# Kernel optimization log

Hardware: AMD Instinct MI355X
Metric: run time of the kernel (lower is better)

## Reference

```python
import jax, jax.numpy as jnp
import numpy as np

BATCH, FRAMES, DIM = 64, 2048, 128
BINS = 1024


def setup_inputs() -> dict:
    key = jax.random.key(0)
    kx, ke = jax.random.split(key)
    x = jax.random.normal(kx, (BATCH, FRAMES, DIM), dtype=jnp.float32)
    embed = jax.random.normal(ke, (BINS, DIM), dtype=jnp.float32)
    return {"x": x, "embed": embed}


def reference(x, embed):
    shape = x.shape
    # preprocess: flatten all leading dims -> [N, D]
    flat = x.reshape(-1, shape[-1])
    # quantize: negative squared euclidean distance, argmax == nearest code
    x_sq = jnp.sum(flat * flat, axis=1, keepdims=True)          # [N, 1]
    e_sq = jnp.sum(embed * embed, axis=1)[None, :]               # [1, BINS]
    dist = -(x_sq - 2.0 * flat @ embed.T + e_sq)                 # [N, BINS]
    embed_ind = jnp.argmax(dist, axis=-1)                        # [N]
    # postprocess: reshape indices to leading dims
    embed_ind = embed_ind.reshape(shape[:-1])                    # [B, T]
    # dequantize: embedding gather
    quantize = embed[embed_ind]                                  # [B, T, D]
    return quantize, embed_ind
```

## Files before the change

### kernel.cpp

```cpp
#include <hip/hip_runtime.h>


#define N_ROWS (64 * 2048)
#define DIM 128
#define BINS 1024
#define MARGIN 0.10f

typedef __attribute__((ext_vector_type(8))) _Float16 half8;
typedef __attribute__((ext_vector_type(4))) float f32x4;

__device__ __forceinline__ void glds16(const void* g, void* l) {
    __builtin_amdgcn_global_load_lds((const __attribute__((address_space(1))) char*)g,
                                     (__attribute__((address_space(3))) char*)l, 16, 0, 0);
}

__global__ __launch_bounds__(256) void prep_kernel(const float* __restrict__ embed,
                                                   _Float16* __restrict__ e_img,
                                                   float* __restrict__ esq_g,
                                                   int* __restrict__ counter) {
    int bin = blockIdx.x * 256 + threadIdx.x;
    if (bin == 0) *counter = 0;
    const float4* e4 = (const float4*)(embed + (size_t)bin * DIM);
    int c = bin >> 8, b = bin & 255;
    float s = 0.f;
#pragma unroll
    for (int g = 0; g < 16; ++g) {
        float4 v0 = e4[2 * g], v1 = e4[2 * g + 1];
        s += v0.x * v0.x + v0.y * v0.y + v0.z * v0.z + v0.w * v0.w;
        s += v1.x * v1.x + v1.y * v1.y + v1.z * v1.z + v1.w * v1.w;
        float f[8] = {v0.x, v0.y, v0.z, v0.w, v1.x, v1.y, v1.z, v1.w};
        half8 H;
#pragma unroll
        for (int j = 0; j < 8; ++j) H[j] = (_Float16)f[j];
        int ks = g >> 2, g2 = g & 3;
        size_t off = ((size_t)(c * 4 + ks) << 14) + (size_t)b * 64 + 16 * (g2 ^ ((b >> 2) & 3));
        *(half8*)((char*)e_img + off) = H;
    }
    esq_g[bin] = s;
}

__global__ __launch_bounds__(1024) __attribute__((amdgpu_waves_per_eu(4, 4)))
void vq_mfma_kernel(const float* __restrict__ x,
                    const _Float16* __restrict__ e_img,
                    const float* __restrict__ esq_g,
                    const float* __restrict__ embed,
                    float* __restrict__ out_idx,
                    float* __restrict__ out_q,
                    int* __restrict__ list,
                    int* __restrict__ counter) {
    __shared__ __align__(16) char smem[53248];
    float* esq_s = (float*)(smem + 49152);

    const int t = threadIdx.x;
    const int wv = t >> 6, lane = t & 63, q = lane >> 4, L15 = lane & 15;
    const int h = wv >> 2, bq = wv & 3;
    const int R0 = blockIdx.x * 128;

    {
        esq_s[t] = esq_g[t];
        const float4* xg = (const float4*)(x + (size_t)R0 * DIM);
#pragma unroll
        for (int qq = 0; qq < 2; ++qq) {
            int G = qq * 1024 + t;
            int row = G >> 4, g = G & 15;
            float4 v0 = xg[row * 32 + 2 * g];
            float4 v1 = xg[row * 32 + 2 * g + 1];
            float f[8] = {v0.x, v0.y, v0.z, v0.w, v1.x, v1.y, v1.z, v1.w};
            half8 H;
#pragma unroll
            for (int j = 0; j < 8; ++j) H[j] = (_Float16)f[j];
            int off = row * 256 + 16 * (g ^ (row & 7));
            *(half8*)(smem + off) = H;
        }
    }
    __syncthreads();

    half8 bh[4][2];
    const int rbase = (32 * h + L15) * 256;
#pragma unroll
    for (int ks = 0; ks < 4; ++ks) {
        const int sB = 16 * ((((ks << 2) | q)) ^ (L15 & 7));
#pragma unroll
        for (int nt = 0; nt < 2; ++nt)
            bh[ks][nt] = *(const half8*)(smem + rbase + nt * 4096 + sB);
    }
    __syncthreads();

    const int aOff = (64 * bq + L15) * 64 + 16 * (q ^ ((L15 >> 2) & 3));

    {
        const char* src = (const char*)e_img;
        const int off = wv << 10;
#pragma unroll
        for (int st = 0; st < 2; ++st)
            glds16(src + ((size_t)st << 14) + off + lane * 16, smem + st * 16384 + off);
        asm volatile("s_waitcnt vmcnt(1)" ::: "memory");
    }
    __builtin_amdgcn_s_barrier();
    asm volatile("" ::: "memory");

    float best[2], sec[2];
    int bidx[2];
#pragma unroll
    for (int nt = 0; nt < 2; ++nt) { best[nt] = -3.4e38f; sec[nt] = -3.4e38f; bidx[nt] = 0; }

    for (int c = 0; c < 4; ++c) {
        f32x4 acc[4][2];
#pragma unroll
        for (int mt = 0; mt < 4; ++mt) {
            f32x4 e2v = *(const f32x4*)&esq_s[256 * c + 64 * bq + 16 * mt + 4 * q];
            f32x4 init;
#pragma unroll
            for (int r = 0; r < 4; ++r) init[r] = -0.5f * e2v[r];
            acc[mt][0] = init;
            acc[mt][1] = init;
        }

#pragma unroll
        for (int s = 0; s < 4; ++s) {
            const int gs = c * 4 + s;
            if (gs < 14) {
                const char* src = (const char*)e_img + ((size_t)(gs + 2) << 14);
                char* dst = smem + ((gs + 2) % 3) * 16384;
                const int off = wv << 10;
                glds16(src + off + lane * 16, dst + off);
            }
            const char* buf = smem + (gs % 3) * 16384;
            half8 a[4];
#pragma unroll
            for (int mt = 0; mt < 4; ++mt)
                a[mt] = *(const half8*)(buf + aOff + mt * 1024);
#pragma unroll
            for (int mt = 0; mt < 4; ++mt)
#pragma unroll
                for (int nt = 0; nt < 2; ++nt)
                    acc[mt][nt] = __builtin_amdgcn_mfma_f32_16x16x32_f16(a[mt], bh[s][nt], acc[mt][nt], 0, 0, 0);
            if (gs < 14) {
                asm volatile("s_waitcnt vmcnt(1)" ::: "memory");
            } else if (gs == 14) {
                asm volatile("s_waitcnt vmcnt(0)" ::: "memory");
            }
            __builtin_amdgcn_s_barrier();
            asm volatile("" ::: "memory");
        }

#pragma unroll
        for (int mt = 0; mt < 4; ++mt)
#pragma unroll
            for (int r = 0; r < 4; ++r) {
                int bin = 256 * c + 64 * bq + 16 * mt + 4 * q + r;
#pragma unroll
                for (int nt = 0; nt < 2; ++nt) {
                    float sc = acc[mt][nt][r];
                    bool gt = sc > best[nt];
                    sec[nt] = __builtin_amdgcn_fmed3f(sc, best[nt], sec[nt]);
                    best[nt] = gt ? sc : best[nt];
                    bidx[nt] = gt ? bin : bidx[nt];
                }
            }
    }

#pragma unroll
    for (int nt = 0; nt < 2; ++nt) {
        for (int off = 16; off <= 32; off <<= 1) {
            float ob = __shfl_xor(best[nt], off);
            float os = __shfl_xor(sec[nt], off);
            int oi = __shfl_xor(bidx[nt], off);
            if (ob > best[nt]) { sec[nt] = fmaxf(best[nt], os); best[nt] = ob; bidx[nt] = oi; }
            else sec[nt] = fmaxf(sec[nt], ob);
        }
    }
    __syncthreads();
    float* sv = (float*)smem;
    int* fidx = (int*)(smem + 8192);
    if (q == 0) {
#pragma unroll
        for (int nt = 0; nt < 2; ++nt) {
            int base = (wv * 32 + 16 * nt + L15) * 3;
            sv[base] = best[nt]; sv[base + 1] = sec[nt];
            ((int*)sv)[base + 2] = bidx[nt];
        }
    }
    __syncthreads();
    if (t < 128) {
        int hh = t >> 5, r32 = t & 31;
        int base0 = ((4 * hh) * 32 + r32) * 3;
        float b0 = sv[base0], s0 = sv[base0 + 1];
        int i0 = ((int*)sv)[base0 + 2];
        for (int w = 1; w < 4; ++w) {
            int base = ((4 * hh + w) * 32 + r32) * 3;
            float ob = sv[base], os = sv[base + 1];
            int oi = ((int*)sv)[base + 2];
            if (ob > b0) { s0 = fmaxf(b0, os); b0 = ob; i0 = oi; }
            else s0 = fmaxf(s0, ob);
        }
        out_idx[R0 + t] = (float)i0;
        fidx[t] = i0;
        if (b0 - s0 < 0.5f * MARGIN) {
            int pos = atomicAdd(counter, 1);
            list[pos] = R0 + t;
        }
    }
    __syncthreads();

    {
        const float4* eg = (const float4*)embed;
        float4* og = (float4*)(out_q + (size_t)R0 * DIM);
#pragma unroll
        for (int i = 0; i < 4; ++i) {
            int f = i * 1024 + t;
            int r = f >> 5, cc = f & 31;
            og[(size_t)r * 32 + cc] = eg[(size_t)fidx[r] * 32 + cc];
        }
    }
}

#define SWB(r, c4) ((r) * 128 + 4 * ((c4) ^ ((r) & 31)))
__global__ __launch_bounds__(256) void refine_kernel(const float* __restrict__ x,
                                                     const float* __restrict__ embed,
                                                     const float* __restrict__ esq_g,
                                                     float* __restrict__ out_idx,
                                                     float* __restrict__ out_q,
                                                     const int* __restrict__ list,
                                                     const int* __restrict__ counter) {
    __shared__ float xr[16 * 128];
    __shared__ float bs[64 * 128];
    __shared__ int rowbuf[16];
    __shared__ int ridx[16];

    const int t = threadIdx.x;
    const int tx = t & 63;
    const int ty = t >> 6;
    const int F = *counter;

    for (int tile = blockIdx.x; tile * 16 < F; tile += gridDim.x) {
        const int base = tile * 16;
        __syncthreads();
        if (t < 16) rowbuf[t] = list[min(base + t, F - 1)];
        __syncthreads();
#pragma unroll
        for (int i = 0; i < 2; ++i) {
            int f = i * 256 + t;
            int r = f >> 5, cc = f & 31;
            float4 v = ((const float4*)(x + (size_t)rowbuf[r] * DIM))[cc];
            *(float4*)&xr[r * 128 + cc * 4] = v;
        }

        float bb[4]; int bi[4];
#pragma unroll
        for (int rr = 0; rr < 4; ++rr) { bb[rr] = -3.4e38f; bi[rr] = 0; }

        for (int chunk = 0; chunk < 16; ++chunk) {
            __syncthreads();
            const float4* eg = (const float4*)(embed + (size_t)chunk * 64 * DIM);
#pragma unroll
            for (int i = 0; i < 8; ++i) {
                int f = i * 256 + t;
                int r = f >> 5, cc = f & 31;
                float4 v = eg[f];
                *(float4*)&bs[SWB(r, cc)] = v;
            }
            __syncthreads();

            float acc[4];
#pragma unroll
            for (int rr = 0; rr < 4; ++rr) acc[rr] = 0.f;
#pragma unroll 8
            for (int k4 = 0; k4 < 32; ++k4) {
                float4 b = *(const float4*)&bs[SWB(tx, k4)];
#pragma unroll
                for (int rr = 0; rr < 4; ++rr) {
                    float4 a = *(const float4*)&xr[(4 * ty + rr) * 128 + k4 * 4];
                    acc[rr] = fmaf(a.x, b.x, acc[rr]);
                    acc[rr] = fmaf(a.y, b.y, acc[rr]);
                    acc[rr] = fmaf(a.z, b.z, acc[rr]);
                    acc[rr] = fmaf(a.w, b.w, acc[rr]);
                }
            }
            const int bin = chunk * 64 + tx;
            const float e2 = esq_g[bin];
#pragma unroll
            for (int rr = 0; rr < 4; ++rr) {
                float sc = 2.f * acc[rr] - e2;
                if (sc > bb[rr]) { bb[rr] = sc; bi[rr] = bin; }
            }
        }

        __syncthreads();
        float* vals = bs;
        int* idxs = (int*)(bs + 1024);
#pragma unroll
        for (int rr = 0; rr < 4; ++rr) {
            vals[(4 * ty + rr) * 64 + tx] = bb[rr];
            idxs[(4 * ty + rr) * 64 + tx] = bi[rr];
        }
        __syncthreads();
        if (t < 16) {
            float bv = vals[t * 64];
            int bix = idxs[t * 64];
            for (int j = 1; j < 64; ++j) {
                float v = vals[t * 64 + j];
                int id = idxs[t * 64 + j];
                if (v > bv || (v == bv && id < bix)) { bv = v; bix = id; }
            }
            ridx[t] = bix;
            if (base + t < F) out_idx[rowbuf[t]] = (float)bix;
        }
        __syncthreads();
        {
            const float4* eg = (const float4*)embed;
#pragma unroll
            for (int i = 0; i < 2; ++i) {
                int f = i * 256 + t;
                int r = f >> 5, cc = f & 31;
                float4* og = (float4*)(out_q + (size_t)rowbuf[r] * DIM);
                og[cc] = eg[(size_t)ridx[r] * 32 + cc];
            }
        }
    }
}

extern "C" void kernel_launch(void* const* d_in, const int* in_sizes, int n_in,
                              void* d_out, int out_size, void* d_ws, size_t ws_size,
                              hipStream_t stream) {
    const float* x = (const float*)d_in[0];
    const float* embed = (const float*)d_in[1];
    float* out_q = (float*)d_out;
    float* out_idx = out_q + (size_t)N_ROWS * DIM;
    char* wsb = (char*)d_ws;
    _Float16* e_img = (_Float16*)wsb;
    float* esq_g = (float*)(wsb + (16 << 14));
    int* counter = (int*)(wsb + (16 << 14) + 4096);
    int* list = (int*)(wsb + (16 << 14) + 4096 + 128);

    prep_kernel<<<BINS / 256, 256, 0, stream>>>(embed, e_img, esq_g, counter);
    vq_mfma_kernel<<<N_ROWS / 128, 1024, 0, stream>>>(x, e_img, esq_g, embed,
                                                      out_idx, out_q, list, counter);
    refine_kernel<<<1024, 256, 0, stream>>>(x, embed, esq_g, out_idx, out_q, list, counter);
}
```

Baseline: 253.7 us.

## Load codebook fragments directly from global memory instead of LDS pipeline

Reorders the fp16 codebook image so that each wave's MFMA A-operand fragment sits contiguously in global memory, and reads those fragments straight into registers instead of staging them through a triple-buffered LDS ring with barriers. Blocks shrink from 1024 threads and 128 rows to 512 threads and 64 rows with much less shared memory, and the forced waves-per-EU attribute is removed. This drops per-step barriers and LDS traffic and should raise occupancy, at the cost of relying on L2/L1 for codebook reuse and exposing global-load latency to the MFMA loop.

```diff
diff --git a/kernel.cpp b/kernel.cpp
--- a/kernel.cpp
+++ b/kernel.cpp
@@ -8,11 +8,6 @@
 
 typedef __attribute__((ext_vector_type(8))) _Float16 half8;
 typedef __attribute__((ext_vector_type(4))) float f32x4;
-
-__device__ __forceinline__ void glds16(const void* g, void* l) {
-    __builtin_amdgcn_global_load_lds((const __attribute__((address_space(1))) char*)g,
-                                     (__attribute__((address_space(3))) char*)l, 16, 0, 0);
-}
 
 __global__ __launch_bounds__(256) void prep_kernel(const float* __restrict__ embed,
                                                    _Float16* __restrict__ e_img,
@@ -22,6 +17,7 @@
     if (bin == 0) *counter = 0;
     const float4* e4 = (const float4*)(embed + (size_t)bin * DIM);
     int c = bin >> 8, b = bin & 255;
+    int bq = b >> 6, mt = (b >> 4) & 3, L15 = b & 15;
     float s = 0.f;
 #pragma unroll
     for (int g = 0; g < 16; ++g) {
@@ -32,14 +28,14 @@
         half8 H;
 #pragma unroll
         for (int j = 0; j < 8; ++j) H[j] = (_Float16)f[j];
-        int ks = g >> 2, g2 = g & 3;
-        size_t off = ((size_t)(c * 4 + ks) << 14) + (size_t)b * 64 + 16 * (g2 ^ ((b >> 2) & 3));
+        int gs = c * 4 + (g >> 2), q = g & 3;
+        size_t off = ((size_t)(((gs * 4 + bq) * 4) + mt) << 10) + (size_t)((q * 16 + L15) << 4);
         *(half8*)((char*)e_img + off) = H;
     }
     esq_g[bin] = s;
 }
 
-__global__ __launch_bounds__(1024) __attribute__((amdgpu_waves_per_eu(4, 4)))
+__global__ __launch_bounds__(512)
 void vq_mfma_kernel(const float* __restrict__ x,
                     const _Float16* __restrict__ e_img,
                     const float* __restrict__ esq_g,
@@ -48,20 +44,21 @@
                     float* __restrict__ out_q,
                     int* __restrict__ list,
                     int* __restrict__ counter) {
-    __shared__ __align__(16) char smem[53248];
-    float* esq_s = (float*)(smem + 49152);
+    __shared__ __align__(16) char smem[20480];
+    float* esq_s = (float*)(smem + 16384);
 
     const int t = threadIdx.x;
     const int wv = t >> 6, lane = t & 63, q = lane >> 4, L15 = lane & 15;
     const int h = wv >> 2, bq = wv & 3;
-    const int R0 = blockIdx.x * 128;
+    const int R0 = blockIdx.x * 64;
 
     {
         esq_s[t] = esq_g[t];
+        esq_s[t + 512] = esq_g[t + 512];
         const float4* xg = (const float4*)(x + (size_t)R0 * DIM);
 #pragma unroll
         for (int qq = 0; qq < 2; ++qq) {
-            int G = qq * 1024 + t;
+            int G = qq * 512 + t;
             int row = G >> 4, g = G & 15;
             float4 v0 = xg[row * 32 + 2 * g];
             float4 v1 = xg[row * 32 + 2 * g + 1];
@@ -84,20 +81,8 @@
         for (int nt = 0; nt < 2; ++nt)
             bh[ks][nt] = *(const half8*)(smem + rbase + nt * 4096 + sB);
     }
-    __syncthreads();
-
-    const int aOff = (64 * bq + L15) * 64 + 16 * (q ^ ((L15 >> 2) & 3));
-
-    {
-        const char* src = (const char*)e_img;
-        const int off = wv << 10;
-#pragma unroll
-        for (int st = 0; st < 2; ++st)
-            glds16(src + ((size_t)st << 14) + off + lane * 16, smem + st * 16384 + off);
-        asm volatile("s_waitcnt vmcnt(1)" ::: "memory");
-    }
-    __builtin_amdgcn_s_barrier();
-    asm volatile("" ::: "memory");
+
+    const char* ebase = (const char*)e_img + (bq << 12) + (lane << 4);
 
     float best[2], sec[2];
     int bidx[2];
@@ -118,30 +103,16 @@
 
 #pragma unroll
         for (int s = 0; s < 4; ++s) {
-            const int gs = c * 4 + s;
-            if (gs < 14) {
-                const char* src = (const char*)e_img + ((size_t)(gs + 2) << 14);
-                char* dst = smem + ((gs + 2) % 3) * 16384;
-                const int off = wv << 10;
-                glds16(src + off + lane * 16, dst + off);
-            }
-            const char* buf = smem + (gs % 3) * 16384;
+            const char* sb = ebase + (((size_t)(c * 4 + s)) << 14);
             half8 a[4];
 #pragma unroll
             for (int mt = 0; mt < 4; ++mt)
-                a[mt] = *(const half8*)(buf + aOff + mt * 1024);
+                a[mt] = *(const half8*)(sb + mt * 1024);
 #pragma unroll
             for (int mt = 0; mt < 4; ++mt)
 #pragma unroll
                 for (int nt = 0; nt < 2; ++nt)
                     acc[mt][nt] = __builtin_amdgcn_mfma_f32_16x16x32_f16(a[mt], bh[s][nt], acc[mt][nt], 0, 0, 0);
-            if (gs < 14) {
-                asm volatile("s_waitcnt vmcnt(1)" ::: "memory");
-            } else if (gs == 14) {
-                asm volatile("s_waitcnt vmcnt(0)" ::: "memory");
-            }
-            __builtin_amdgcn_s_barrier();
-            asm volatile("" ::: "memory");
         }
 
 #pragma unroll
@@ -172,7 +143,7 @@
     }
     __syncthreads();
     float* sv = (float*)smem;
-    int* fidx = (int*)(smem + 8192);
+    int* fidx = (int*)(smem + 4096);
     if (q == 0) {
 #pragma unroll
         for (int nt = 0; nt < 2; ++nt) {
@@ -182,7 +153,7 @@
         }
     }
     __syncthreads();
-    if (t < 128) {
+    if (t < 64) {
         int hh = t >> 5, r32 = t & 31;
         int base0 = ((4 * hh) * 32 + r32) * 3;
         float b0 = sv[base0], s0 = sv[base0 + 1];
@@ -208,7 +179,7 @@
         float4* og = (float4*)(out_q + (size_t)R0 * DIM);
 #pragma unroll
         for (int i = 0; i < 4; ++i) {
-            int f = i * 1024 + t;
+            int f = i * 512 + t;
             int r = f >> 5, cc = f & 31;
             og[(size_t)r * 32 + cc] = eg[(size_t)fidx[r] * 32 + cc];
         }
@@ -334,7 +305,7 @@
     int* list = (int*)(wsb + (16 << 14) + 4096 + 128);
 
     prep_kernel<<<BINS / 256, 256, 0, stream>>>(embed, e_img, esq_g, counter);
-    vq_mfma_kernel<<<N_ROWS / 128, 1024, 0, stream>>>(x, e_img, esq_g, embed,
-                                                      out_idx, out_q, list, counter);
+    vq_mfma_kernel<<<N_ROWS / 64, 512, 0, stream>>>(x, e_img, esq_g, embed,
+                                                    out_idx, out_q, list, counter);
     refine_kernel<<<1024, 256, 0, stream>>>(x, embed, esq_g, out_idx, out_q, list, counter);
 }
```

New measurement: 237.6 us. 1.07x faster.
